# Performance work log

Measured on AMD Instinct MI355X. Metric: run time of the kernel, lower is better.

Reference implementation:

```python
import jax, jax.numpy as jnp
import numpy as np

EMBED_DIM = 768
FF_DIM = 3072
NUM_EXPERTS = 8
TOP_K = 2
CAPACITY_FACTOR = 1.25  # training-mode capacity factor
LB_WEIGHT = 0.01
Z_WEIGHT = 0.001


def setup_inputs() -> dict:
    key = jax.random.key(0)
    k0, k1, k2, k3, k4 = jax.random.split(key, 5)
    B, S, D, F, E = 4, 2048, EMBED_DIM, FF_DIM, NUM_EXPERTS
    scale_d = 1.0 / np.sqrt(D)
    scale_f = 1.0 / np.sqrt(F)
    return {
        "x": jax.random.normal(k0, (B, S, D), dtype=jnp.float32),
        # router gate: nn.Linear(D, E, bias=False) -> weight [E, D]
        "w_gate": jax.random.normal(k1, (E, D), dtype=jnp.float32) * scale_d,
        # stacked expert weights, torch Linear layout [out, in]
        "wi_gate": jax.random.normal(k2, (E, F, D), dtype=jnp.float32) * scale_d,
        "wi_up": jax.random.normal(k3, (E, F, D), dtype=jnp.float32) * scale_d,
        "wo": jax.random.normal(k4, (E, D, F), dtype=jnp.float32) * scale_f,
    }


def moe_forward(x, w_gate, wi_gate, wi_up, wo):
    B, S, D = x.shape
    E = w_gate.shape[0]
    K = TOP_K
    T = B * S
    capacity = max(int(T * K / E * CAPACITY_FACTOR), K)

    xf = x.reshape(T, D)
    router_logits = xf @ w_gate.T                        # [T, E]
    router_probs = jax.nn.softmax(router_logits, axis=-1)
    topk_probs, topk_idx = jax.lax.top_k(router_probs, K)  # [T, K]
    topk_probs = topk_probs / topk_probs.sum(axis=-1, keepdims=True)

    # one-hot dispatch mask [T, K, E]
    onehot = (topk_idx[:, :, None] == jnp.arange(E)[None, None, :]).astype(xf.dtype)
    # per-(k, expert) arrival rank of each token (torch truncates first `capacity`
    # tokens in token-index order, independently per k and per expert)
    rank = ((jnp.cumsum(onehot, axis=0) - onehot) * onehot).sum(-1)  # [T, K]
    keep = (rank < capacity).astype(xf.dtype)                        # [T, K]

    # combine weights per (token, expert) [T, E]
    combine = jnp.einsum('tk,tk,tke->te', topk_probs, keep, onehot)

    out = jnp.zeros_like(xf)
    for e in range(E):  # fixed small structural loop over experts
        gate = jax.nn.silu(xf @ wi_gate[e].T)   # [T, F]
        up = xf @ wi_up[e].T                    # [T, F]
        y = (gate * up) @ wo[e].T               # [T, D]
        out = out + y * combine[:, e:e + 1]

    # auxiliary losses
    expert_mask = onehot.sum(axis=1)            # [T, E]
    f = expert_mask.sum(axis=0) / (T * K)
    P = router_probs.mean(axis=0)
    load_balance_loss = E * (f * P).sum()
    z_loss = jnp.mean(jax.nn.logsumexp(router_logits, axis=-1) ** 2)
    aux_loss = LB_WEIGHT * load_balance_loss + Z_WEIGHT * z_loss

    return out.reshape(B, S, D), aux_loss


def reference(x, w_gate, wi_gate, wi_up, wo):
    return moe_forward(x, w_gate, wi_gate, wi_up, wo)
```

## Files before the change

kernel.cpp:

```cpp
#include <hip/hip_runtime.h>

typedef unsigned short u16;
typedef unsigned int u32;
typedef unsigned long long u64;

#define T_TOK 8192
#define DIM 768
#define FF 3072
#define NE 8
#define CAP 2560
#define LSTR 5120
#define MAXMT 20
#define N8EACH 2359296
#define NCAST2 18432
#define NWOCAST 2304

typedef __attribute__((ext_vector_type(8))) short s8v;
typedef __attribute__((ext_vector_type(4))) float f4v;

__device__ __forceinline__ u16 f2bf(float f) {
  union { float f; u32 u; } v; v.f = f;
  u32 r = v.u + 0x7FFFu + ((v.u >> 16) & 1u);
  return (u16)(r >> 16);
}

__device__ __forceinline__ void glds16(const void* g, void* l) {
  __builtin_amdgcn_global_load_lds(
      (const __attribute__((address_space(1))) u32*)g,
      (__attribute__((address_space(3))) u32*)l, 16, 0, 0);
}

__device__ __forceinline__ void cast8(const float* __restrict__ s, u16* __restrict__ d, int j) {
  const float4* s4 = (const float4*)s;
  float4 a = s4[2 * j], b = s4[2 * j + 1];
  uint4 o;
  o.x = (u32)f2bf(a.x) | ((u32)f2bf(a.y) << 16);
  o.y = (u32)f2bf(a.z) | ((u32)f2bf(a.w) << 16);
  o.z = (u32)f2bf(b.x) | ((u32)f2bf(b.y) << 16);
  o.w = (u32)f2bf(b.z) | ((u32)f2bf(b.w) << 16);
  ((uint4*)d)[j] = o;
}

__global__ __launch_bounds__(256) void pre_kernel(
    const float* __restrict__ wig, const float* __restrict__ wiu,
    u16* __restrict__ wgb, u16* __restrict__ wub,
    const float* __restrict__ x, const float* __restrict__ wg, u16* __restrict__ xb,
    int* __restrict__ tki, float* __restrict__ tkp,
    float* __restrict__ probs, float* __restrict__ lse2, int* __restrict__ ctrl) {
  int bid = blockIdx.x;
  if (bid == 0 && threadIdx.x < 64) ctrl[threadIdx.x] = 0;
  if (bid < NCAST2) {
    int i = bid * 256 + threadIdx.x;
    if (i < N8EACH) cast8(wig, wgb, i);
    else cast8(wiu, wub, i - N8EACH);
    return;
  }
  int rb = bid - NCAST2;
  int lane = threadIdx.x & 63;
  int t = rb * 4 + (threadIdx.x >> 6);
  const float* xr = x + (long)t * DIM;
  u16* xw = xb + (long)t * DIM;
  float acc[NE];
#pragma unroll
  for (int e = 0; e < NE; e++) acc[e] = 0.f;
  for (int i = 0; i < DIM / 64; i++) {
    float xv = xr[lane + 64 * i];
    xw[lane + 64 * i] = f2bf(xv);
#pragma unroll
    for (int e = 0; e < NE; e++) acc[e] += xv * wg[e * DIM + lane + 64 * i];
  }
#pragma unroll
  for (int off = 32; off > 0; off >>= 1) {
#pragma unroll
    for (int e = 0; e < NE; e++) acc[e] += __shfl_xor(acc[e], off);
  }
  if (lane == 0) {
    float m = acc[0];
#pragma unroll
    for (int e = 1; e < NE; e++) m = fmaxf(m, acc[e]);
    float p[NE], s = 0.f;
#pragma unroll
    for (int e = 0; e < NE; e++) { p[e] = __expf(acc[e] - m); s += p[e]; }
    float inv = 1.f / s;
    int e0 = 0;
#pragma unroll
    for (int e = 1; e < NE; e++) if (acc[e] > acc[e0]) e0 = e;
    int e1 = (e0 == 0) ? 1 : 0;
#pragma unroll
    for (int e = 0; e < NE; e++) if (e != e0 && acc[e] > acc[e1]) e1 = e;
    float p0 = p[e0] * inv, p1 = p[e1] * inv;
    float rn = 1.f / (p0 + p1);
    tki[2 * t] = e0; tki[2 * t + 1] = e1;
    tkp[2 * t] = p0 * rn; tkp[2 * t + 1] = p1 * rn;
    float4 pa = {p[0] * inv, p[1] * inv, p[2] * inv, p[3] * inv};
    float4 pb = {p[4] * inv, p[5] * inv, p[6] * inv, p[7] * inv};
    ((float4*)(probs + t * 8))[0] = pa;
    ((float4*)(probs + t * 8))[1] = pb;
    float lse = __logf(s) + m;
    lse2[t] = lse * lse;
  }
}

__global__ __launch_bounds__(1024) void rankred_kernel(
    const int* __restrict__ tki, const float* __restrict__ tkp,
    const float* __restrict__ probs, const float* __restrict__ lse2,
    int* __restrict__ ltk, float* __restrict__ lw,
    int* __restrict__ counts, int* __restrict__ baserow, int* __restrict__ kflags,
    int* __restrict__ fcnt, float* __restrict__ psum, float* __restrict__ zsum,
    const float* __restrict__ wo, u16* __restrict__ wob) {
  int bid = blockIdx.x;
  int tid = threadIdx.x;
  if (bid >= 9) {
    int j = (bid - 9) * 1024 + tid;
    cast8(wo, wob, j);
    return;
  }
  if (bid >= 1) {
    int t = (bid - 1) * 1024 + tid;
    float4 pa = ((const float4*)(probs + t * 8))[0];
    float4 pb = ((const float4*)(probs + t * 8))[1];
    float p[8] = {pa.x, pa.y, pa.z, pa.w, pb.x, pb.y, pb.z, pb.w};
    float z = lse2[t];
    int e0 = tki[2 * t], e1 = tki[2 * t + 1];
    int fc[8];
#pragma unroll
    for (int e = 0; e < 8; e++) fc[e] = (e0 == e ? 1 : 0) + (e1 == e ? 1 : 0);
#pragma unroll
    for (int off = 32; off > 0; off >>= 1) {
#pragma unroll
      for (int e = 0; e < 8; e++) { p[e] += __shfl_xor(p[e], off); fc[e] += __shfl_xor(fc[e], off); }
      z += __shfl_xor(z, off);
    }
    __shared__ float sp[16][9];
    __shared__ int sf[16][8];
    int wv = tid >> 6, lane = tid & 63;
    if (lane == 0) {
#pragma unroll
      for (int e = 0; e < 8; e++) { sp[wv][e] = p[e]; sf[wv][e] = fc[e]; }
      sp[wv][8] = z;
    }
    __syncthreads();
    if (tid < 9) {
      float s = 0.f;
      for (int w = 0; w < 16; w++) s += sp[w][tid];
      if (tid < 8) atomicAdd(&psum[tid], s);
      else atomicAdd(zsum, s);
    }
    if (tid >= 64 && tid < 72) {
      int e = tid - 64;
      int s = 0;
      for (int w = 0; w < 16; w++) s += sf[w][e];
      atomicAdd(&fcnt[e], s);
    }
    return;
  }
  __shared__ int wave_cnt[2][16][8];
  __shared__ int base[2][8];
  __shared__ int sc0[8];
  int wv = tid >> 6, lane = tid & 63;
  int c0w[8];
#pragma unroll
  for (int e = 0; e < 8; e++) c0w[e] = 0;
  for (int c = 0; c < T_TOK / 1024; c++) {
    int e0 = tki[2 * (c * 1024 + tid)];
#pragma unroll
    for (int e = 0; e < 8; e++) {
      u64 m = __ballot(e0 == e);
      if (lane == 0) c0w[e] += __popcll(m);
    }
  }
  if (lane == 0) {
#pragma unroll
    for (int e = 0; e < 8; e++) wave_cnt[0][wv][e] = c0w[e];
  }
  if (tid < 16) base[tid >> 3][tid & 7] = 0;
  __syncthreads();
  if (tid < 8) {
    int s = 0;
    for (int w = 0; w < 16; w++) s += wave_cnt[0][w][tid];
    sc0[tid] = (s < CAP) ? s : CAP;
  }
  __syncthreads();
  u64 lmask = (lane == 63) ? 0x7FFFFFFFFFFFFFFFull : ((1ull << lane) - 1ull);
  for (int c = 0; c < T_TOK / 1024; c++) {
    int t = c * 1024 + tid;
    int e0 = tki[2 * t], e1 = tki[2 * t + 1];
    float p0 = tkp[2 * t], p1 = tkp[2 * t + 1];
    int pre0 = 0, pre1 = 0;
    for (int e = 0; e < 8; e++) {
      u64 m0 = __ballot(e0 == e);
      if (e0 == e) pre0 = __popcll(m0 & lmask);
      if (lane == 0) wave_cnt[0][wv][e] = __popcll(m0);
      u64 m1 = __ballot(e1 == e);
      if (e1 == e) pre1 = __popcll(m1 & lmask);
      if (lane == 0) wave_cnt[1][wv][e] = __popcll(m1);
    }
    __syncthreads();
    if (tid < 16) {
      int k = tid >> 3, e = tid & 7;
      int run = base[k][e];
      for (int w = 0; w < 16; w++) {
        int v = wave_cnt[k][w][e];
        wave_cnt[k][w][e] = run;
        run += v;
      }
      base[k][e] = run;
    }
    __syncthreads();
    int r0 = wave_cnt[0][wv][e0] + pre0;
    int r1 = wave_cnt[1][wv][e1] + pre1;
    if (r0 < CAP) { ltk[e0 * LSTR + r0] = (t << 1); lw[e0 * LSTR + r0] = p0; }
    if (r1 < CAP) {
      int p = sc0[e1] + r1;
      ltk[e1 * LSTR + p] = (t << 1) | 1; lw[e1 * LSTR + p] = p1;
    }
    kflags[t] = (r0 < CAP ? 1 : 0) | (r1 < CAP ? 2 : 0);
    __syncthreads();
  }
  if (tid == 0) {
    int run = 0;
    for (int e = 0; e < 8; e++) {
      int c1 = base[1][e]; if (c1 > CAP) c1 = CAP;
      int cnt = sc0[e] + c1;
      counts[e] = cnt; baserow[e] = run; run += cnt;
    }
  }
}

__global__ __launch_bounds__(256, 2) void gemm1_kernel(
    const u16* __restrict__ xb, const u16* __restrict__ wgb, const u16* __restrict__ wub,
    u16* __restrict__ H, const int* __restrict__ counts, const int* __restrict__ baserow,
    const int* __restrict__ ltk) {
  int id = blockIdx.x;
  int xcd = id & 7;
  int q = id >> 3;
  int gg = q / MAXMT;
  int mt = q - gg * MAXMT;
  int g = gg * 8 + xcd;
  int e = g / 48;
  int nt = g - e * 48;
  int cnt = counts[e];
  if (mt * 128 >= cnt) return;

  __shared__ u16 As[128 * 64];
  __shared__ u16 Bg[64 * 64];
  __shared__ u16 Bu[64 * 64];
  __shared__ int toks[128];
  int tid = threadIdx.x;
  if (tid < 128) {
    int r = mt * 128 + tid; if (r > cnt - 1) r = cnt - 1;
    toks[tid] = ltk[e * LSTR + r] >> 1;
  }
  __syncthreads();
  int rq8 = tid >> 3;
  int swz = ((tid & 7) ^ (rq8 & 7)) * 8;
  long tA0 = toks[rq8], tA1 = toks[32 + rq8], tA2 = toks[64 + rq8], tA3 = toks[96 + rq8];
  const u16* gA0 = xb + tA0 * DIM + swz;
  const u16* gA1 = xb + tA1 * DIM + swz;
  const u16* gA2 = xb + tA2 * DIM + swz;
  const u16* gA3 = xb + tA3 * DIM + swz;
  long bO0 = ((long)e * FF + nt * 64 + rq8) * DIM + swz;
  long bO1 = bO0 + 32l * DIM;
  const u16* gG0 = wgb + bO0; const u16* gG1 = wgb + bO1;
  const u16* gU0 = wub + bO0; const u16* gU1 = wub + bO1;
  u16* dA0 = As + tid * 8; u16* dA1 = dA0 + 2048; u16* dA2 = dA0 + 4096; u16* dA3 = dA0 + 6144;
  u16* dG0 = Bg + tid * 8; u16* dG1 = dG0 + 2048;
  u16* dU0 = Bu + tid * 8; u16* dU1 = dU0 + 2048;

  int lane = tid & 63, wv = tid >> 6;
  int wm = (wv & 1) * 64, wn = (wv >> 1) * 32;
  int lrow = lane & 15, quad = lane >> 4;
  int sl0 = (quad ^ (lrow & 7)) * 8;
  int sl1 = ((quad + 4) ^ (lrow & 7)) * 8;

  f4v zero = {0.f, 0.f, 0.f, 0.f};
  f4v accg[4][2], accu[4][2];
#pragma unroll
  for (int i = 0; i < 4; i++)
#pragma unroll
    for (int j = 0; j < 2; j++) { accg[i][j] = zero; accu[i][j] = zero; }

  for (int kt = 0; kt < DIM / 64; kt++) {
    int ko = kt * 64;
    __syncthreads();
    glds16(gA0 + ko, dA0); glds16(gA1 + ko, dA1);
    glds16(gA2 + ko, dA2); glds16(gA3 + ko, dA3);
    glds16(gG0 + ko, dG0); glds16(gG1 + ko, dG1);
    glds16(gU0 + ko, dU0); glds16(gU1 + ko, dU1);
    __syncthreads();
#pragma unroll
    for (int kk = 0; kk < 2; kk++) {
      int sl = kk ? sl1 : sl0;
      s8v a[4], bgf[2], buf[2];
#pragma unroll
      for (int i = 0; i < 4; i++)
        a[i] = *(const s8v*)&As[(wm + i * 16 + lrow) * 64 + sl];
#pragma unroll
      for (int j = 0; j < 2; j++) {
        bgf[j] = *(const s8v*)&Bg[(wn + j * 16 + lrow) * 64 + sl];
        buf[j] = *(const s8v*)&Bu[(wn + j * 16 + lrow) * 64 + sl];
      }
#pragma unroll
      for (int i = 0; i < 4; i++)
#pragma unroll
        for (int j = 0; j < 2; j++) {
          accg[i][j] = __builtin_amdgcn_mfma_f32_16x16x32_bf16(a[i], bgf[j], accg[i][j], 0, 0, 0);
          accu[i][j] = __builtin_amdgcn_mfma_f32_16x16x32_bf16(a[i], buf[j], accu[i][j], 0, 0, 0);
        }
    }
  }
  long hb = (long)baserow[e] + (long)mt * 128;
#pragma unroll
  for (int i = 0; i < 4; i++) {
#pragma unroll
    for (int r = 0; r < 4; r++) {
      int m = wm + i * 16 + quad * 4 + r;
      if (mt * 128 + m < cnt) {
#pragma unroll
        for (int j = 0; j < 2; j++) {
          float gv = accg[i][j][r], uv = accu[i][j][r];
          float h = gv / (1.f + __expf(-gv)) * uv;
          H[(hb + m) * FF + nt * 64 + wn + j * 16 + lrow] = f2bf(h);
        }
      }
    }
  }
}

__global__ __launch_bounds__(256, 2) void gemm2_kernel(
    const u16* __restrict__ H, const u16* __restrict__ wob,
    float* __restrict__ ybuf, const int* __restrict__ counts, const int* __restrict__ baserow,
    const int* __restrict__ ltk, const float* __restrict__ lw) {
  int id = blockIdx.x;
  int xcd = id & 7;
  int q = id >> 3;
  int gg = q / 6;
  int nt = q - gg * 6;
  int g = gg * 8 + xcd;
  int e = g / MAXMT;
  int mt = g - e * MAXMT;
  int cnt = counts[e];
  if (mt * 128 >= cnt) return;

  __shared__ u16 As[128 * 64];
  __shared__ u16 Bs[128 * 64];
  __shared__ int stok[128];
  __shared__ float sw[128];
  int tid = threadIdx.x;
  if (tid < 128) {
    int r = mt * 128 + tid; if (r > cnt - 1) r = cnt - 1;
    stok[tid] = ltk[e * LSTR + r];
    sw[tid] = lw[e * LSTR + r];
  }
  long hb = (long)baserow[e] + (long)mt * 128;
  int rq8 = tid >> 3;
  int swz = ((tid & 7) ^ (rq8 & 7)) * 8;
  const u16* gA0 = H + (hb + rq8) * FF + swz;
  const u16* gA1 = gA0 + 32l * FF;
  const u16* gA2 = gA0 + 64l * FF;
  const u16* gA3 = gA0 + 96l * FF;
  long bOff = ((long)e * DIM + nt * 128 + rq8) * FF + swz;
  const u16* gB0 = wob + bOff;
  const u16* gB1 = gB0 + 32l * FF;
  const u16* gB2 = gB0 + 64l * FF;
  const u16* gB3 = gB0 + 96l * FF;
  u16* dA0 = As + tid * 8; u16* dA1 = dA0 + 2048; u16* dA2 = dA0 + 4096; u16* dA3 = dA0 + 6144;
  u16* dB0 = Bs + tid * 8; u16* dB1 = dB0 + 2048; u16* dB2 = dB0 + 4096; u16* dB3 = dB0 + 6144;
  int lane = tid & 63, wv = tid >> 6;
  int wm = (wv & 1) * 64, wn = (wv >> 1) * 64;
  int lrow = lane & 15, quad = lane >> 4;
  int sl0 = (quad ^ (lrow & 7)) * 8;
  int sl1 = ((quad + 4) ^ (lrow & 7)) * 8;
  f4v zero = {0.f, 0.f, 0.f, 0.f};
  f4v acc[4][4];
#pragma unroll
  for (int i = 0; i < 4; i++)
#pragma unroll
    for (int j = 0; j < 4; j++) acc[i][j] = zero;

  for (int kt = 0; kt < FF / 64; kt++) {
    int ko = kt * 64;
    __syncthreads();
    glds16(gA0 + ko, dA0); glds16(gA1 + ko, dA1);
    glds16(gA2 + ko, dA2); glds16(gA3 + ko, dA3);
    glds16(gB0 + ko, dB0); glds16(gB1 + ko, dB1);
    glds16(gB2 + ko, dB2); glds16(gB3 + ko, dB3);
    __syncthreads();
#pragma unroll
    for (int kk = 0; kk < 2; kk++) {
      int sl = kk ? sl1 : sl0;
      s8v a[4], b[4];
#pragma unroll
      for (int i = 0; i < 4; i++)
        a[i] = *(const s8v*)&As[(wm + i * 16 + lrow) * 64 + sl];
#pragma unroll
      for (int j = 0; j < 4; j++)
        b[j] = *(const s8v*)&Bs[(wn + j * 16 + lrow) * 64 + sl];
#pragma unroll
      for (int i = 0; i < 4; i++)
#pragma unroll
        for (int j = 0; j < 4; j++)
          acc[i][j] = __builtin_amdgcn_mfma_f32_16x16x32_bf16(a[i], b[j], acc[i][j], 0, 0, 0);
    }
  }
#pragma unroll
  for (int i = 0; i < 4; i++) {
#pragma unroll
    for (int r = 0; r < 4; r++) {
      int m = wm + i * 16 + quad * 4 + r;
      if (mt * 128 + m < cnt) {
        int entry = stok[m];
        float w = sw[m];
        long ob = (long)entry * DIM + nt * 128;
#pragma unroll
        for (int j = 0; j < 4; j++)
          ybuf[ob + wn + j * 16 + lrow] = acc[i][j][r] * w;
      }
    }
  }
}

__global__ __launch_bounds__(256) void combine_aux_kernel(
    const float* __restrict__ ybuf, const int* __restrict__ kflags, float* __restrict__ out,
    const int* __restrict__ fcnt, const float* __restrict__ psum, const float* __restrict__ zsum) {
  int bid = blockIdx.x;
  if (bid == T_TOK * DIM / 4 / 256) {
    if (threadIdx.x == 0) {
      float lb = 0.f;
      for (int e = 0; e < 8; e++)
        lb += ((float)fcnt[e] / (float)(T_TOK * 2)) * (psum[e] / (float)T_TOK);
      lb *= 8.f;
      float z = zsum[0] / (float)T_TOK;
      out[(size_t)T_TOK * DIM] = 0.01f * lb + 0.001f * z;
    }
    return;
  }
  int idx = bid * 256 + threadIdx.x;
  int t = idx / (DIM / 4);
  int d4 = idx - t * (DIM / 4);
  int kf = kflags[t];
  float4 r = {0.f, 0.f, 0.f, 0.f};
  if (kf & 1) {
    float4 a = ((const float4*)(ybuf + (long)(2 * t) * DIM))[d4];
    r.x += a.x; r.y += a.y; r.z += a.z; r.w += a.w;
  }
  if (kf & 2) {
    float4 b = ((const float4*)(ybuf + (long)(2 * t + 1) * DIM))[d4];
    r.x += b.x; r.y += b.y; r.z += b.z; r.w += b.w;
  }
  ((float4*)out)[idx] = r;
}

extern "C" void kernel_launch(void* const* d_in, const int* in_sizes, int n_in,
                              void* d_out, int out_size, void* d_ws, size_t ws_size,
                              hipStream_t stream) {
  const float* x = (const float*)d_in[0];
  const float* wgate = (const float*)d_in[1];
  const float* wig = (const float*)d_in[2];
  const float* wiu = (const float*)d_in[3];
  const float* wo = (const float*)d_in[4];
  float* out = (float*)d_out;

  char* ws = (char*)d_ws;
  size_t off = 0;
  auto alloc = [&](size_t bytes) {
    void* p = ws + off;
    off += (bytes + 255) & ~(size_t)255;
    return p;
  };
  int* ctrl = (int*)alloc(256);
  u16* xb = (u16*)alloc((size_t)T_TOK * DIM * 2);
  u16* wgb = (u16*)alloc((size_t)NE * FF * DIM * 2);
  u16* wub = (u16*)alloc((size_t)NE * FF * DIM * 2);
  u16* wob = (u16*)alloc((size_t)NE * DIM * FF * 2);
  u16* Hbuf = (u16*)alloc((size_t)(T_TOK * 2 + 128) * FF * 2);
  int* tki = (int*)alloc((size_t)T_TOK * 2 * 4);
  float* tkp = (float*)alloc((size_t)T_TOK * 2 * 4);
  int* ltk = (int*)alloc((size_t)NE * LSTR * 4);
  float* lw = (float*)alloc((size_t)NE * LSTR * 4);
  float* probs = (float*)alloc((size_t)T_TOK * 8 * 4);
  float* lse2 = (float*)alloc((size_t)T_TOK * 4);
  int* kflags = (int*)alloc((size_t)T_TOK * 4);
  float* ybuf = (float*)wgb;

  int* fcnt = ctrl;
  int* counts = ctrl + 8;
  int* baserow = ctrl + 16;
  float* psum = (float*)(ctrl + 24);
  float* zsum = (float*)(ctrl + 32);

  pre_kernel<<<NCAST2 + T_TOK / 4, 256, 0, stream>>>(
      wig, wiu, wgb, wub, x, wgate, xb, tki, tkp, probs, lse2, ctrl);
  rankred_kernel<<<9 + NWOCAST, 1024, 0, stream>>>(
      tki, tkp, probs, lse2, ltk, lw, counts, baserow, kflags, fcnt, psum, zsum, wo, wob);
  gemm1_kernel<<<8 * 48 * MAXMT, 256, 0, stream>>>(xb, wgb, wub, Hbuf, counts, baserow, ltk);
  gemm2_kernel<<<8 * MAXMT * 6, 256, 0, stream>>>(Hbuf, wob, ybuf, counts, baserow, ltk, lw);
  combine_aux_kernel<<<T_TOK * DIM / 4 / 256 + 1, 256, 0, stream>>>(
      ybuf, kflags, out, fcnt, psum, zsum);
}
```

Baseline: 551.7 us.

## Parallelize capacity ranking per (expert,k) block and move wo cast into gemm1

The single-block rank/scatter loop that handled all experts and both top-k slots is split into 16 blocks, one per (expert, k) pair, each doing a ballot prefix scan over tokens. Per-expert counts and base rows are now computed inside the GEMM kernels from per-(k,e) counts. The fp32-to-bf16 cast of wo moves from the rank kernel into extra tail blocks of gemm1, so the ranking kernel no longer waits behind the cast. The intent is to remove a serial single-block bottleneck, at the cost of redundant reads of tki and a second kflags array.

```diff
diff --git a/kernel.cpp b/kernel.cpp
--- a/kernel.cpp
+++ b/kernel.cpp
@@ -13,6 +13,7 @@
 #define MAXMT 20
 #define N8EACH 2359296
 #define NCAST2 18432
+#define G1BLK 7680
 #define NWOCAST 2304
 
 typedef __attribute__((ext_vector_type(8))) short s8v;
@@ -40,6 +41,7 @@
   o.w = (u32)f2bf(b.z) | ((u32)f2bf(b.w) << 16);
   ((uint4*)d)[j] = o;
 }
+
 
 __global__ __launch_bounds__(256) void pre_kernel(
     const float* __restrict__ wig, const float* __restrict__ wiu,
@@ -104,19 +106,13 @@
 __global__ __launch_bounds__(1024) void rankred_kernel(
     const int* __restrict__ tki, const float* __restrict__ tkp,
     const float* __restrict__ probs, const float* __restrict__ lse2,
-    int* __restrict__ ltk, float* __restrict__ lw,
-    int* __restrict__ counts, int* __restrict__ baserow, int* __restrict__ kflags,
-    int* __restrict__ fcnt, float* __restrict__ psum, float* __restrict__ zsum,
-    const float* __restrict__ wo, u16* __restrict__ wob) {
+    int* __restrict__ ltk, float* __restrict__ lw, int* __restrict__ ctrl,
+    int* __restrict__ kflags0, int* __restrict__ kflags1) {
   int bid = blockIdx.x;
   int tid = threadIdx.x;
-  if (bid >= 9) {
-    int j = (bid - 9) * 1024 + tid;
-    cast8(wo, wob, j);
-    return;
-  }
-  if (bid >= 1) {
-    int t = (bid - 1) * 1024 + tid;
+  int wv = tid >> 6, lane = tid & 63;
+  if (bid >= 16) {
+    int t = (bid - 16) * 1024 + tid;
     float4 pa = ((const float4*)(probs + t * 8))[0];
     float4 pb = ((const float4*)(probs + t * 8))[1];
     float p[8] = {pa.x, pa.y, pa.z, pa.w, pb.x, pb.y, pb.z, pb.w};
@@ -133,13 +129,14 @@
     }
     __shared__ float sp[16][9];
     __shared__ int sf[16][8];
-    int wv = tid >> 6, lane = tid & 63;
     if (lane == 0) {
 #pragma unroll
       for (int e = 0; e < 8; e++) { sp[wv][e] = p[e]; sf[wv][e] = fc[e]; }
       sp[wv][8] = z;
     }
     __syncthreads();
+    float* psum = (float*)(ctrl + 24);
+    float* zsum = (float*)(ctrl + 32);
     if (tid < 9) {
       float s = 0.f;
       for (int w = 0; w < 16; w++) s += sp[w][tid];
@@ -150,88 +147,91 @@
       int e = tid - 64;
       int s = 0;
       for (int w = 0; w < 16; w++) s += sf[w][e];
-      atomicAdd(&fcnt[e], s);
+      atomicAdd(&ctrl[e], s);
     }
     return;
   }
-  __shared__ int wave_cnt[2][16][8];
-  __shared__ int base[2][8];
-  __shared__ int sc0[8];
-  int wv = tid >> 6, lane = tid & 63;
-  int c0w[8];
-#pragma unroll
-  for (int e = 0; e < 8; e++) c0w[e] = 0;
-  for (int c = 0; c < T_TOK / 1024; c++) {
-    int e0 = tki[2 * (c * 1024 + tid)];
-#pragma unroll
-    for (int e = 0; e < 8; e++) {
+  int k = bid & 1, e = bid >> 1;
+  __shared__ int wcnt[16];
+  __shared__ int runbase;
+  __shared__ int s_sc0;
+  u64 lmask = (lane == 63) ? 0x7FFFFFFFFFFFFFFFull : ((1ull << lane) - 1ull);
+  int sc0 = 0;
+  if (k == 1) {
+    int c0 = 0;
+    for (int c = 0; c < T_TOK / 1024; c++) {
+      int e0 = tki[2 * (c * 1024 + tid)];
       u64 m = __ballot(e0 == e);
-      if (lane == 0) c0w[e] += __popcll(m);
-    }
-  }
-  if (lane == 0) {
-#pragma unroll
-    for (int e = 0; e < 8; e++) wave_cnt[0][wv][e] = c0w[e];
-  }
-  if (tid < 16) base[tid >> 3][tid & 7] = 0;
+      if (lane == 0) c0 += __popcll(m);
+    }
+    if (lane == 0) wcnt[wv] = c0;
+    __syncthreads();
+    if (tid == 0) {
+      int s = 0;
+      for (int w = 0; w < 16; w++) s += wcnt[w];
+      s_sc0 = (s < CAP) ? s : CAP;
+    }
+    __syncthreads();
+    sc0 = s_sc0;
+  }
+  if (tid == 0) runbase = 0;
   __syncthreads();
-  if (tid < 8) {
-    int s = 0;
-    for (int w = 0; w < 16; w++) s += wave_cnt[0][w][tid];
-    sc0[tid] = (s < CAP) ? s : CAP;
-  }
-  __syncthreads();
-  u64 lmask = (lane == 63) ? 0x7FFFFFFFFFFFFFFFull : ((1ull << lane) - 1ull);
   for (int c = 0; c < T_TOK / 1024; c++) {
     int t = c * 1024 + tid;
-    int e0 = tki[2 * t], e1 = tki[2 * t + 1];
-    float p0 = tkp[2 * t], p1 = tkp[2 * t + 1];
-    int pre0 = 0, pre1 = 0;
-    for (int e = 0; e < 8; e++) {
-      u64 m0 = __ballot(e0 == e);
-      if (e0 == e) pre0 = __popcll(m0 & lmask);
-      if (lane == 0) wave_cnt[0][wv][e] = __popcll(m0);
-      u64 m1 = __ballot(e1 == e);
-      if (e1 == e) pre1 = __popcll(m1 & lmask);
-      if (lane == 0) wave_cnt[1][wv][e] = __popcll(m1);
-    }
-    __syncthreads();
-    if (tid < 16) {
-      int k = tid >> 3, e = tid & 7;
-      int run = base[k][e];
-      for (int w = 0; w < 16; w++) {
-        int v = wave_cnt[k][w][e];
-        wave_cnt[k][w][e] = run;
-        run += v;
+    int ek = tki[2 * t + k];
+    float pk = tkp[2 * t + k];
+    u64 m = __ballot(ek == e);
+    int pre = __popcll(m & lmask);
+    if (lane == 0) wcnt[wv] = __popcll(m);
+    __syncthreads();
+    int waveoff = runbase;
+    for (int w = 0; w < wv; w++) waveoff += wcnt[w];
+    int r = waveoff + pre;
+    if (ek == e) {
+      int keep = (r < CAP) ? 1 : 0;
+      if (keep) {
+        int p = sc0 + r;
+        ltk[e * LSTR + p] = (t << 1) | k;
+        lw[e * LSTR + p] = pk;
       }
-      base[k][e] = run;
-    }
-    __syncthreads();
-    int r0 = wave_cnt[0][wv][e0] + pre0;
-    int r1 = wave_cnt[1][wv][e1] + pre1;
-    if (r0 < CAP) { ltk[e0 * LSTR + r0] = (t << 1); lw[e0 * LSTR + r0] = p0; }
-    if (r1 < CAP) {
-      int p = sc0[e1] + r1;
-      ltk[e1 * LSTR + p] = (t << 1) | 1; lw[e1 * LSTR + p] = p1;
-    }
-    kflags[t] = (r0 < CAP ? 1 : 0) | (r1 < CAP ? 2 : 0);
+      if (k == 0) kflags0[t] = keep; else kflags1[t] = keep;
+    }
+    __syncthreads();
+    if (tid == 0) {
+      int tot = 0;
+      for (int w = 0; w < 16; w++) tot += wcnt[w];
+      runbase += tot;
+    }
     __syncthreads();
   }
   if (tid == 0) {
-    int run = 0;
-    for (int e = 0; e < 8; e++) {
-      int c1 = base[1][e]; if (c1 > CAP) c1 = CAP;
-      int cnt = sc0[e] + c1;
-      counts[e] = cnt; baserow[e] = run; run += cnt;
-    }
+    int cnt = runbase; if (cnt > CAP) cnt = CAP;
+    ctrl[8 + k * 8 + e] = cnt;
+  }
+}
+
+__device__ __forceinline__ void expert_extent(const int* __restrict__ ctrl, int e,
+                                              int& cnt, long& hb0) {
+  cnt = 0; hb0 = 0;
+#pragma unroll
+  for (int i = 0; i < 8; i++) {
+    int ci = ctrl[8 + i] + ctrl[16 + i];
+    if (i < e) hb0 += ci;
+    if (i == e) cnt = ci;
   }
 }
 
 __global__ __launch_bounds__(256, 2) void gemm1_kernel(
     const u16* __restrict__ xb, const u16* __restrict__ wgb, const u16* __restrict__ wub,
-    u16* __restrict__ H, const int* __restrict__ counts, const int* __restrict__ baserow,
-    const int* __restrict__ ltk) {
+    u16* __restrict__ H, const int* __restrict__ ctrl, const int* __restrict__ ltk,
+    const float* __restrict__ wo, u16* __restrict__ wob) {
   int id = blockIdx.x;
+  if (id >= G1BLK) {
+    int base = (id - G1BLK) * 1024 + threadIdx.x;
+#pragma unroll
+    for (int c = 0; c < 4; c++) cast8(wo, wob, base + c * 256);
+    return;
+  }
   int xcd = id & 7;
   int q = id >> 3;
   int gg = q / MAXMT;
@@ -239,7 +239,8 @@
   int g = gg * 8 + xcd;
   int e = g / 48;
   int nt = g - e * 48;
-  int cnt = counts[e];
+  int cnt; long hb0;
+  expert_extent(ctrl, e, cnt, hb0);
   if (mt * 128 >= cnt) return;
 
   __shared__ u16 As[128 * 64];
@@ -309,7 +310,7 @@
         }
     }
   }
-  long hb = (long)baserow[e] + (long)mt * 128;
+  long hb = hb0 + (long)mt * 128;
 #pragma unroll
   for (int i = 0; i < 4; i++) {
 #pragma unroll
@@ -329,7 +330,7 @@
 
 __global__ __launch_bounds__(256, 2) void gemm2_kernel(
     const u16* __restrict__ H, const u16* __restrict__ wob,
-    float* __restrict__ ybuf, const int* __restrict__ counts, const int* __restrict__ baserow,
+    float* __restrict__ ybuf, const int* __restrict__ ctrl,
     const int* __restrict__ ltk, const float* __restrict__ lw) {
   int id = blockIdx.x;
   int xcd = id & 7;
@@ -339,7 +340,8 @@
   int g = gg * 8 + xcd;
   int e = g / MAXMT;
   int mt = g - e * MAXMT;
-  int cnt = counts[e];
+  int cnt; long hb0;
+  expert_extent(ctrl, e, cnt, hb0);
   if (mt * 128 >= cnt) return;
 
   __shared__ u16 As[128 * 64];
@@ -352,7 +354,7 @@
     stok[tid] = ltk[e * LSTR + r];
     sw[tid] = lw[e * LSTR + r];
   }
-  long hb = (long)baserow[e] + (long)mt * 128;
+  long hb = hb0 + (long)mt * 128;
   int rq8 = tid >> 3;
   int swz = ((tid & 7) ^ (rq8 & 7)) * 8;
   const u16* gA0 = H + (hb + rq8) * FF + swz;
@@ -421,14 +423,17 @@
 }
 
 __global__ __launch_bounds__(256) void combine_aux_kernel(
-    const float* __restrict__ ybuf, const int* __restrict__ kflags, float* __restrict__ out,
-    const int* __restrict__ fcnt, const float* __restrict__ psum, const float* __restrict__ zsum) {
+    const float* __restrict__ ybuf, const int* __restrict__ kflags0,
+    const int* __restrict__ kflags1, float* __restrict__ out,
+    const int* __restrict__ ctrl) {
   int bid = blockIdx.x;
   if (bid == T_TOK * DIM / 4 / 256) {
     if (threadIdx.x == 0) {
+      const float* psum = (const float*)(ctrl + 24);
+      const float* zsum = (const float*)(ctrl + 32);
       float lb = 0.f;
       for (int e = 0; e < 8; e++)
-        lb += ((float)fcnt[e] / (float)(T_TOK * 2)) * (psum[e] / (float)T_TOK);
+        lb += ((float)ctrl[e] / (float)(T_TOK * 2)) * (psum[e] / (float)T_TOK);
       lb *= 8.f;
       float z = zsum[0] / (float)T_TOK;
       out[(size_t)T_TOK * DIM] = 0.01f * lb + 0.001f * z;
@@ -438,13 +443,12 @@
   int idx = bid * 256 + threadIdx.x;
   int t = idx / (DIM / 4);
   int d4 = idx - t * (DIM / 4);
-  int kf = kflags[t];
   float4 r = {0.f, 0.f, 0.f, 0.f};
-  if (kf & 1) {
+  if (kflags0[t]) {
     float4 a = ((const float4*)(ybuf + (long)(2 * t) * DIM))[d4];
     r.x += a.x; r.y += a.y; r.z += a.z; r.w += a.w;
   }
-  if (kf & 2) {
+  if (kflags1[t]) {
     float4 b = ((const float4*)(ybuf + (long)(2 * t + 1) * DIM))[d4];
     r.x += b.x; r.y += b.y; r.z += b.z; r.w += b.w;
   }
@@ -480,21 +484,17 @@
   float* lw = (float*)alloc((size_t)NE * LSTR * 4);
   float* probs = (float*)alloc((size_t)T_TOK * 8 * 4);
   float* lse2 = (float*)alloc((size_t)T_TOK * 4);
-  int* kflags = (int*)alloc((size_t)T_TOK * 4);
+  int* kflags0 = (int*)alloc((size_t)T_TOK * 4);
+  int* kflags1 = (int*)alloc((size_t)T_TOK * 4);
   float* ybuf = (float*)wgb;
-
-  int* fcnt = ctrl;
-  int* counts = ctrl + 8;
-  int* baserow = ctrl + 16;
-  float* psum = (float*)(ctrl + 24);
-  float* zsum = (float*)(ctrl + 32);
 
   pre_kernel<<<NCAST2 + T_TOK / 4, 256, 0, stream>>>(
       wig, wiu, wgb, wub, x, wgate, xb, tki, tkp, probs, lse2, ctrl);
-  rankred_kernel<<<9 + NWOCAST, 1024, 0, stream>>>(
-      tki, tkp, probs, lse2, ltk, lw, counts, baserow, kflags, fcnt, psum, zsum, wo, wob);
-  gemm1_kernel<<<8 * 48 * MAXMT, 256, 0, stream>>>(xb, wgb, wub, Hbuf, counts, baserow, ltk);
-  gemm2_kernel<<<8 * MAXMT * 6, 256, 0, stream>>>(Hbuf, wob, ybuf, counts, baserow, ltk, lw);
+  rankred_kernel<<<24, 1024, 0, stream>>>(
+      tki, tkp, probs, lse2, ltk, lw, ctrl, kflags0, kflags1);
+  gemm1_kernel<<<G1BLK + NWOCAST, 256, 0, stream>>>(
+      xb, wgb, wub, Hbuf, ctrl, ltk, wo, wob);
+  gemm2_kernel<<<8 * MAXMT * 6, 256, 0, stream>>>(Hbuf, wob, ybuf, ctrl, ltk, lw);
   combine_aux_kernel<<<T_TOK * DIM / 4 / 256 + 1, 256, 0, stream>>>(
-      ybuf, kflags, out, fcnt, psum, zsum);
-}
+      ybuf, kflags0, kflags1, out, ctrl);
+}
```

After: 546.0 us. About the same (-1.0%).
